# Kernel optimization log

Hardware: AMD Instinct MI355X
Metric: run time of the kernel (lower is better)

## Reference

```python
import jax, jax.numpy as jnp
from jax import lax
import numpy as np

# TopoLoss(dim=1, p=2, topo_lambda=1.0)
# p=2 -> Euclidean ground metric for the Vietoris-Rips filtration.
# This reference computes the dominant H0 persistence diagram of the VR complex:
# for a point cloud, H0 births are all 0 and deaths are exactly the MST edge
# weights (Kruskal/union-find == Prim, computed here with a fixed-length scan).
# Wasserstein distance between the two diagrams (equal cardinality N-1, births 0)
# reduces to optimal 1D matching of the sorted death values (q=1, the
# torch_topological WassersteinDistance default).
TOPO_LAMBDA = 1.0
EPS = 1e-12


def _pairwise_euclidean(x):
    # x: [B, N, D] -> [B, N, N] via the Gram trick (avoids [B,N,N,D] temp)
    sq = jnp.sum(x * x, axis=-1)                      # [B, N]
    g = jnp.einsum('bnd,bmd->bnm', x, x)              # [B, N, N]
    d2 = sq[:, :, None] + sq[:, None, :] - 2.0 * g
    return jnp.sqrt(jnp.maximum(d2, 0.0) + EPS)


def _mst_deaths(D):
    # Prim's algorithm on a dense distance matrix D: [N, N].
    # Returns the sorted MST edge weights = H0 death times ([N-1]).
    N = D.shape[0]
    inf = jnp.asarray(jnp.inf, D.dtype)
    in_tree0 = jnp.zeros((N,), bool).at[0].set(True)
    min_dist0 = D[0]

    def step(carry, _):
        in_tree, min_dist = carry
        masked = jnp.where(in_tree, inf, min_dist)
        j = jnp.argmin(masked)
        death = masked[j]
        in_tree = in_tree.at[j].set(True)
        min_dist = jnp.minimum(min_dist, D[j])
        return (in_tree, min_dist), death

    _, deaths = lax.scan(step, (in_tree0, min_dist0), None, length=N - 1)
    return jnp.sort(deaths)


def _h0_diagram_deaths(x):
    # x: [B, N, D] -> sorted death values [B, N-1]
    D = _pairwise_euclidean(x)
    return jax.vmap(_mst_deaths)(D)


def setup_inputs() -> dict:
    key = jax.random.key(0)
    k1, k2 = jax.random.split(key)
    B, N, D = 64, 1024, 3
    gts = jax.random.normal(k1, (B, N, D), dtype=jnp.float32)
    preds = jax.random.normal(k2, (B, N, D), dtype=jnp.float32)
    return {"gts": gts, "preds": preds}


def reference(gts, preds):
    # note: source names pers_info_pred = complex(gts) (vars swapped there);
    # Wasserstein is symmetric so ordering is irrelevant.
    deaths_a = _h0_diagram_deaths(gts)    # [B, N-1]
    deaths_b = _h0_diagram_deaths(preds)  # [B, N-1]
    # W1 between diagrams with equal cardinality and births==0:
    # optimal matching of sorted death coordinates.
    per_batch = jnp.sum(jnp.abs(deaths_a - deaths_b), axis=-1)  # [B]
    return per_batch.mean() * TOPO_LAMBDA
```

## Files before the change

### kernel.cpp

```cpp
#include <hip/hip_runtime.h>
#include <math.h>

#define N 1024
#define T 1024
#define HALF 512
#define PHASE_CAP 10
#define SWITCH 80

typedef float v2f __attribute__((ext_vector_type(2)));
typedef unsigned long long ull;

#define INF64 0xFFFFFFFFFFFFFFFFull
#define INF32 0xFFFFFFFFu

__device__ __forceinline__ unsigned umin32(unsigned a, unsigned b) { return a < b ? a : b; }
__device__ __forceinline__ unsigned umax32(unsigned a, unsigned b) { return a > b ? a : b; }
__device__ __forceinline__ int imin32(int a, int b) { return a < b ? a : b; }

__device__ __forceinline__ unsigned walk_root(const unsigned* parent, unsigned x) {
    unsigned prev = x, cur = parent[x];
    while (cur != prev) {
        unsigned nxt = parent[cur];
        if (nxt == prev) { cur = umin32(cur, prev); break; }
        prev = cur; cur = nxt;
    }
    return cur;
}

#define DPP_MIN_SHR(v, sh)                                                                   \
    do {                                                                                     \
        unsigned _t = (unsigned)__builtin_amdgcn_update_dpp(                                 \
            (int)0xFFFFFFFF, (int)(v), 0x110 | (sh), 0xF, 0xF, false);                       \
        (v) = umin32((v), _t);                                                               \
    } while (0)

__global__ __launch_bounds__(T) void scan1_kernel(const float* __restrict__ gts,
                                                  const float* __restrict__ preds,
                                                  unsigned* __restrict__ bests1) {
    __shared__ float4 p4[N];
    __shared__ unsigned pb8[8][HALF];
    const int t = threadIdx.x;
    const int cloud = blockIdx.x >> 1;
    const int nh = blockIdx.x & 1;
    const float* __restrict__ src = (cloud < 64 ? gts : preds) + (size_t)(cloud & 63) * N * 3;

    {
        float* stg = (float*)&pb8[0][0];
        if (t < 768) ((float4*)stg)[t] = ((const float4*)src)[t];
        __syncthreads();
        p4[t] = make_float4(stg[3 * t], stg[3 * t + 1], stg[3 * t + 2], 0.0f);
        __syncthreads();
    }

    const int q = t & 127;
    const int s = t >> 7;
    const int jbase = s << 7;
    const int n0 = nh * HALF + q;
    const int n1 = n0 + 128, n2 = n0 + 256, n3 = n0 + 384;
    const float4 a0 = p4[n0], a1 = p4[n1], a2 = p4[n2], a3 = p4[n3];
    const v2f axA = (v2f){a0.x, a1.x}, ayA = (v2f){a0.y, a1.y}, azA = (v2f){a0.z, a1.z};
    const v2f axB = (v2f){a2.x, a3.x}, ayB = (v2f){a2.y, a3.y}, azB = (v2f){a2.z, a3.z};
    unsigned b0 = INF32, b1 = INF32, b2 = INF32, b3 = INF32;
    #pragma unroll 4
    for (int jj = 0; jj < 128; jj += 2) {
        const int j = jbase + jj;
        const float4 qa = p4[j];
        const float4 qb = p4[j + 1];
        #define STEP1(QQ, JV)                                                           \
        {                                                                               \
            const v2f sxv = (v2f){QQ.x, QQ.x}, syv = (v2f){QQ.y, QQ.y},                 \
                      szv = (v2f){QQ.z, QQ.z};                                          \
            v2f dxA = axA - sxv, dyA = ayA - syv, dzA = azA - szv;                      \
            v2f eA = dxA * dxA;                                                         \
            eA = __builtin_elementwise_fma(dyA, dyA, eA);                               \
            eA = __builtin_elementwise_fma(dzA, dzA, eA);                               \
            v2f dxB = axB - sxv, dyB = ayB - syv, dzB = azB - szv;                      \
            v2f eB = dxB * dxB;                                                         \
            eB = __builtin_elementwise_fma(dyB, dyB, eB);                               \
            eB = __builtin_elementwise_fma(dzB, dzB, eB);                               \
            unsigned kk;                                                                \
            kk = (__float_as_uint(eA.x) & 0xFFFFF800u) | (unsigned)(JV);                \
            b0 = umin32(b0, ((JV) == n0) ? INF32 : kk);                                 \
            kk = (__float_as_uint(eA.y) & 0xFFFFF800u) | (unsigned)(JV);                \
            b1 = umin32(b1, ((JV) == n1) ? INF32 : kk);                                 \
            kk = (__float_as_uint(eB.x) & 0xFFFFF800u) | (unsigned)(JV);                \
            b2 = umin32(b2, ((JV) == n2) ? INF32 : kk);                                 \
            kk = (__float_as_uint(eB.y) & 0xFFFFF800u) | (unsigned)(JV);                \
            b3 = umin32(b3, ((JV) == n3) ? INF32 : kk);                                 \
        }
        STEP1(qa, j)
        STEP1(qb, j + 1)
        #undef STEP1
    }
    pb8[s][q] = b0; pb8[s][q + 128] = b1; pb8[s][q + 256] = b2; pb8[s][q + 384] = b3;
    __syncthreads();
    if (t < HALF) {
        unsigned best = umin32(umin32(pb8[0][t], pb8[1][t]), umin32(pb8[2][t], pb8[3][t]));
        best = umin32(best, umin32(umin32(pb8[4][t], pb8[5][t]), umin32(pb8[6][t], pb8[7][t])));
        bests1[(size_t)cloud * N + nh * HALF + t] = best;
    }
}

__global__ __launch_bounds__(T) void scan2_kernel(const float* __restrict__ gts,
                                                  const float* __restrict__ preds,
                                                  const unsigned* __restrict__ bests1,
                                                  unsigned* __restrict__ bests2) {
    __shared__ float4 p4[N];
    __shared__ unsigned cw[N];
    __shared__ unsigned parent[N];
    __shared__ unsigned pb8[8][HALF];
    const int t = threadIdx.x;
    const int cloud = blockIdx.x >> 1;
    const int nh = blockIdx.x & 1;
    const float* __restrict__ src = (cloud < 64 ? gts : preds) + (size_t)(cloud & 63) * N * 3;

    {
        float* stg = (float*)&pb8[0][0];
        if (t < 768) ((float4*)stg)[t] = ((const float4*)src)[t];
        __syncthreads();
        p4[t] = make_float4(stg[3 * t], stg[3 * t + 1], stg[3 * t + 2], 0.0f);
    }
    parent[t] = bests1[(size_t)cloud * N + t] & 0x3FFu;
    __syncthreads();
    {
        unsigned r = walk_root(parent, (unsigned)t);
        parent[t] = r;
        cw[t] = r;
    }
    __syncthreads();

    const int q = t & 127;
    const int s = t >> 7;
    const int jbase = s << 7;
    const int n0 = nh * HALF + q;
    const int n1 = n0 + 128, n2 = n0 + 256, n3 = n0 + 384;
    const unsigned c0 = cw[n0], c1 = cw[n1], c2 = cw[n2], c3 = cw[n3];
    const float4 a0 = p4[n0], a1 = p4[n1], a2 = p4[n2], a3 = p4[n3];
    const v2f axA = (v2f){a0.x, a1.x}, ayA = (v2f){a0.y, a1.y}, azA = (v2f){a0.z, a1.z};
    const v2f axB = (v2f){a2.x, a3.x}, ayB = (v2f){a2.y, a3.y}, azB = (v2f){a2.z, a3.z};
    unsigned b0 = INF32, b1 = INF32, b2 = INF32, b3 = INF32;
    #pragma unroll 4
    for (int jj = 0; jj < 128; jj += 2) {
        const int j = jbase + jj;
        const float4 qa = p4[j];
        const float4 qb = p4[j + 1];
        uint2 cj = *(const uint2*)&cw[j];
        #define STEP2(QQ, CJ, JV)                                                       \
        {                                                                               \
            const v2f sxv = (v2f){QQ.x, QQ.x}, syv = (v2f){QQ.y, QQ.y},                 \
                      szv = (v2f){QQ.z, QQ.z};                                          \
            v2f dxA = axA - sxv, dyA = ayA - syv, dzA = azA - szv;                      \
            v2f eA = dxA * dxA;                                                         \
            eA = __builtin_elementwise_fma(dyA, dyA, eA);                               \
            eA = __builtin_elementwise_fma(dzA, dzA, eA);                               \
            v2f dxB = axB - sxv, dyB = ayB - syv, dzB = azB - szv;                      \
            v2f eB = dxB * dxB;                                                         \
            eB = __builtin_elementwise_fma(dyB, dyB, eB);                               \
            eB = __builtin_elementwise_fma(dzB, dzB, eB);                               \
            unsigned kk;                                                                \
            kk = (__float_as_uint(eA.x) & 0xFFFFF800u) | (unsigned)(JV);                \
            b0 = umin32(b0, ((CJ) == c0) ? INF32 : kk);                                 \
            kk = (__float_as_uint(eA.y) & 0xFFFFF800u) | (unsigned)(JV);                \
            b1 = umin32(b1, ((CJ) == c1) ? INF32 : kk);                                 \
            kk = (__float_as_uint(eB.x) & 0xFFFFF800u) | (unsigned)(JV);                \
            b2 = umin32(b2, ((CJ) == c2) ? INF32 : kk);                                 \
            kk = (__float_as_uint(eB.y) & 0xFFFFF800u) | (unsigned)(JV);                \
            b3 = umin32(b3, ((CJ) == c3) ? INF32 : kk);                                 \
        }
        STEP2(qa, cj.x, j)
        STEP2(qb, cj.y, j + 1)
        #undef STEP2
    }
    pb8[s][q] = b0; pb8[s][q + 128] = b1; pb8[s][q + 256] = b2; pb8[s][q + 384] = b3;
    __syncthreads();
    if (t < HALF) {
        unsigned best = umin32(umin32(pb8[0][t], pb8[1][t]), umin32(pb8[2][t], pb8[3][t]));
        best = umin32(best, umin32(umin32(pb8[4][t], pb8[5][t]), umin32(pb8[6][t], pb8[7][t])));
        bests2[(size_t)cloud * N + nh * HALF + t] = best;
    }
}

__global__ __launch_bounds__(T) void final_kernel(const float* __restrict__ gts,
                                                  const float* __restrict__ preds,
                                                  float* __restrict__ ws,
                                                  const unsigned* __restrict__ bests1,
                                                  const unsigned* __restrict__ bests2,
                                                  int nPre) {
    __shared__ float4 pts[N];
    __shared__ float4 spts[N];
    __shared__ unsigned comp[N];
    __shared__ ull bestComp[N];
    __shared__ unsigned parent[N];
    __shared__ __align__(16) unsigned pb[2][N];
    __shared__ float deaths[N];
    __shared__ unsigned wsum[16];
    __shared__ int deathCount;

    const int t = threadIdx.x;
    const int blk = blockIdx.x;
    const float* __restrict__ src = (blk < 64 ? gts : preds) + (size_t)(blk & 63) * N * 3;

    {
        float* stg = (float*)&spts[0];
        if (t < 768) ((float4*)stg)[t] = ((const float4*)src)[t];
        __syncthreads();
        float x = stg[3 * t], y = stg[3 * t + 1], z = stg[3 * t + 2];
        pts[t] = make_float4(x, y, z, __uint_as_float((unsigned)t));
        comp[t] = (unsigned)t;
        parent[t] = (unsigned)t;
        deaths[t] = 0.0f;
        bestComp[t] = INF64;
    }
    if (t == 0) deathCount = 0;
    __syncthreads();

    const int n = t & (HALF - 1);
    const int h = t >> 9;
    const int n2 = n + HALF;
    const int jbase = h * HALF;
    float4 pA = pts[n], pB = pts[n2];
    const v2f pxv = (v2f){pA.x, pB.x};
    const v2f pyv = (v2f){pA.y, pB.y};
    const v2f pzv = (v2f){pA.z, pB.z};

    if (nPre >= 1) {
        unsigned b1 = bests1[(size_t)blk * N + t];
        unsigned j1 = b1 & 0x3FFu;
        unsigned e1 = b1 & 0xFFFFF800u;
        parent[t] = j1;
        __syncthreads();
        {
            unsigned p = j1;
            unsigned gp = parent[p];
            bool mutual = (gp == (unsigned)t);
            bool rec = !mutual || ((unsigned)t < p);
            float dval = rec ? sqrtf(__uint_as_float(e1) + 1e-12f) : 0.0f;
            ull m = __ballot(rec);
            int cnt = __popcll(m);
            int base = 0;
            if ((t & 63) == 0 && cnt) base = atomicAdd(&deathCount, cnt);
            base = __shfl(base, 0, 64);
            if (rec) {
                int idx = base + __popcll(m & ((1ull << (t & 63)) - 1ull));
                if (idx < N - 1) deaths[idx] = dval;
            }
        }
        __syncthreads();
        {
            unsigned r = walk_root(parent, (unsigned)t);
            parent[t] = r;
            comp[t] = r;
            pts[t].w = __uint_as_float(r);
        }
        __syncthreads();
    }

    if (nPre >= 2) {
        unsigned b2 = bests2[(size_t)blk * N + t];
        if (b2 != INF32) {
            unsigned j2 = b2 & 0x3FFu, e2 = b2 & 0xFFFFF800u;
            unsigned mn = umin32((unsigned)t, j2), mx = umax32((unsigned)t, j2);
            atomicMin(&bestComp[comp[t]], ((ull)e2 << 20) | (ull)((mn << 10) | mx));
        }
        __syncthreads();
        const unsigned c = (unsigned)t;
        const bool isRoot = (parent[c] == c);
        {
            ull bc = bestComp[c];
            if (isRoot && bc != INF64) {
                unsigned mn = (unsigned)((bc >> 10) & 0x3FFu);
                unsigned mx = (unsigned)(bc & 0x3FFu);
                unsigned cm = comp[mn];
                parent[c] = (cm == c) ? comp[mx] : cm;
            }
        }
        __syncthreads();
        {
            bool rec = false;
            float dval = 0.0f;
            unsigned p = parent[c];
            if (isRoot && p != c) {
                unsigned gp = parent[p];
                bool mutual = (gp == c);
                rec = !mutual || (c < p);
                if (rec) dval = sqrtf(__uint_as_float((unsigned)(bestComp[c] >> 20)) + 1e-12f);
            }
            ull m = __ballot(rec);
            int cnt = __popcll(m);
            int base = 0;
            if ((t & 63) == 0 && cnt) base = atomicAdd(&deathCount, cnt);
            base = __shfl(base, 0, 64);
            if (rec) {
                int idx = base + __popcll(m & ((1ull << (t & 63)) - 1ull));
                if (idx < N - 1) deaths[idx] = dval;
            }
        }
        __syncthreads();
        {
            unsigned r = walk_root(parent, c);
            parent[t] = r;
            unsigned nc = walk_root(parent, comp[t]);
            comp[t] = nc;
            pts[t].w = __uint_as_float(nc);
            bestComp[t] = INF64;
        }
        __syncthreads();
    }

    int phase = nPre;
    while (N - deathCount > (nPre ? SWITCH : 1) && phase < PHASE_CAP) {
        const unsigned c0 = comp[n], c1 = comp[n2];
        unsigned best0 = INF32, best1 = INF32;
        #pragma unroll 8
        for (int jj = 0; jj < HALF; ++jj) {
            int j = jbase + jj;
            float4 pj = pts[j];
            unsigned cj = __float_as_uint(pj.w);
            v2f dx = pxv - (v2f){pj.x, pj.x};
            v2f dy = pyv - (v2f){pj.y, pj.y};
            v2f dz = pzv - (v2f){pj.z, pj.z};
            v2f e = dx * dx;
            e = __builtin_elementwise_fma(dy, dy, e);
            e = __builtin_elementwise_fma(dz, dz, e);
            unsigned k0 = (__float_as_uint(e.x) & 0xFFFFF800u) | (unsigned)j;
            unsigned k1 = (__float_as_uint(e.y) & 0xFFFFF800u) | (unsigned)j;
            k0 = (cj == c0) ? INF32 : k0;
            k1 = (cj == c1) ? INF32 : k1;
            best0 = umin32(best0, k0);
            best1 = umin32(best1, k1);
        }
        pb[h][n] = best0;
        pb[h][n2] = best1;
        __syncthreads();
        if (h == 0) {
            #pragma unroll
            for (int s = 0; s < 2; ++s) {
                int m = s == 0 ? n : n2;
                unsigned fb = umin32(pb[0][m], pb[1][m]);
                if (fb != INF32) {
                    unsigned j = fb & 0x3FFu, e = fb & 0xFFFFF800u;
                    unsigned mn = umin32((unsigned)m, j), mx = umax32((unsigned)m, j);
                    ull key = ((ull)e << 20) | (ull)((mn << 10) | mx);
                    if (phase == 0) bestComp[m] = key;
                    else atomicMin(&bestComp[comp[m]], key);
                }
            }
        }
        __syncthreads();
        const unsigned c = (unsigned)t;
        const bool isRoot = (parent[c] == c);
        {
            ull bc = bestComp[c];
            if (isRoot && bc != INF64) {
                unsigned mn = (unsigned)((bc >> 10) & 0x3FFu);
                unsigned mx = (unsigned)(bc & 0x3FFu);
                unsigned cm = comp[mn];
                parent[c] = (cm == c) ? comp[mx] : cm;
            }
        }
        __syncthreads();
        {
            bool rec = false;
            float dval = 0.0f;
            unsigned p = parent[c];
            if (isRoot && p != c) {
                unsigned gp = parent[p];
                bool mutual = (gp == c);
                rec = !mutual || (c < p);
                if (rec) dval = sqrtf(__uint_as_float((unsigned)(bestComp[c] >> 20)) + 1e-12f);
            }
            ull m = __ballot(rec);
            int cnt = __popcll(m);
            int base = 0;
            if ((t & 63) == 0 && cnt) base = atomicAdd(&deathCount, cnt);
            base = __shfl(base, 0, 64);
            if (rec) {
                int idx = base + __popcll(m & ((1ull << (t & 63)) - 1ull));
                if (idx < N - 1) deaths[idx] = dval;
            }
        }
        __syncthreads();
        {
            unsigned r = walk_root(parent, c);
            parent[t] = r;
            unsigned nc = walk_root(parent, comp[t]);
            comp[t] = nc;
            pts[t].w = __uint_as_float(nc);
            bestComp[t] = INF64;
        }
        __syncthreads();
        ++phase;
    }

    const int dcbase = deathCount;
    const int comps = N - dcbase;
    if (comps > 1) {
        unsigned* scomp = &pb[0][0];
        unsigned* hist = &pb[1][0];
        unsigned* wavemin = &pb[1][0];
        uint2* segs = (uint2*)&bestComp[0];
        const int lane = t & 63;
        const int wid = t >> 6;

        hist[t] = 0;
        __syncthreads();
        atomicAdd(&hist[comp[t]], 1u);
        __syncthreads();
        unsigned cnt = hist[t];
        unsigned inc = cnt;
        #pragma unroll
        for (int d = 1; d < 64; d <<= 1) {
            unsigned u = __shfl_up(inc, d, 64);
            if (lane >= d) inc += u;
        }
        if (lane == 63) wsum[wid] = inc;
        __syncthreads();
        unsigned wof = 0;
        for (int i = 0; i < wid; ++i) wof += wsum[i];
        unsigned excl = wof + inc - cnt;
        if (cnt) { segs[t].x = excl; segs[t].y = excl + cnt; }
        __syncthreads();
        hist[t] = excl;
        __syncthreads();
        {
            unsigned pos = atomicAdd(&hist[comp[t]], 1u);
            spts[pos] = pts[t];
            scomp[pos] = comp[t];
        }
        __syncthreads();

        unsigned c_cur = comp[0];
        v2f pxv2 = (v2f){0.f, 0.f}, pyv2 = pxv2, pzv2 = pxv2;
        unsigned myc0 = 0, myc1 = 0, md0 = INF32, md1 = INF32;
        if (t < HALF) {
            float4 q0 = spts[t], q1 = spts[t + HALF];
            myc0 = scomp[t];
            myc1 = scomp[t + HALF];
            pxv2 = (v2f){q0.x, q1.x};
            pyv2 = (v2f){q0.y, q1.y};
            pzv2 = (v2f){q0.z, q1.z};
            if (myc0 == c_cur) pxv2.x = INFINITY;
            if (myc1 == c_cur) pxv2.y = INFINITY;
        }

        for (int step = 0; step < comps - 1; ++step) {
            if (t < HALF) {
                uint2 sg = segs[c_cur];
                const int jb = (int)sg.x, je = (int)sg.y, jl = je - 1;
                for (int base = jb; base < je; base += 4) {
                    float4 q0 = spts[base];
                    float4 q1 = spts[imin32(base + 1, jl)];
                    float4 q2 = spts[imin32(base + 2, jl)];
                    float4 q3 = spts[imin32(base + 3, jl)];
                    #define RELAX(qq)                                                        \
                        {                                                                    \
                            v2f dx = pxv2 - (v2f){qq.x, qq.x};                               \
                            v2f dy = pyv2 - (v2f){qq.y, qq.y};                               \
                            v2f dz = pzv2 - (v2f){qq.z, qq.z};                               \
                            v2f e = dx * dx;                                                 \
                            e = __builtin_elementwise_fma(dy, dy, e);                        \
                            e = __builtin_elementwise_fma(dz, dz, e);                        \
                            md0 = umin32(md0, (__float_as_uint(e.x) & 0xFFFFFC00u) | myc0);  \
                            md1 = umin32(md1, (__float_as_uint(e.y) & 0xFFFFFC00u) | myc1);  \
                        }
                    RELAX(q0) RELAX(q1) RELAX(q2) RELAX(q3)
                    #undef RELAX
                }
                unsigned v = umin32(md0, md1);
                DPP_MIN_SHR(v, 1);
                DPP_MIN_SHR(v, 2);
                DPP_MIN_SHR(v, 4);
                DPP_MIN_SHR(v, 8);
                unsigned r0 = (unsigned)__builtin_amdgcn_readlane((int)v, 15);
                unsigned r1 = (unsigned)__builtin_amdgcn_readlane((int)v, 31);
                unsigned r2 = (unsigned)__builtin_amdgcn_readlane((int)v, 47);
                unsigned r3 = (unsigned)__builtin_amdgcn_readlane((int)v, 63);
                if (lane == 0)
                    wavemin[(step & 1) * 8 + wid] = umin32(umin32(r0, r1), umin32(r2, r3));
            }
            __syncthreads();
            if (t < HALF) {
                const uint4* wmv = (const uint4*)(wavemin + (step & 1) * 8);
                uint4 u0 = wmv[0], u1 = wmv[1];
                unsigned m0 = umin32(umin32(u0.x, u0.y), umin32(u0.z, u0.w));
                unsigned m1 = umin32(umin32(u1.x, u1.y), umin32(u1.z, u1.w));
                unsigned G = umin32(m0, m1);
                c_cur = G & 0x3FFu;
                if (t == 0)
                    deaths[dcbase + step] = sqrtf(__uint_as_float(G & 0xFFFFFC00u) + 1e-12f);
                if (myc0 == c_cur) { pxv2.x = INFINITY; md0 = INF32; }
                if (myc1 == c_cur) { pxv2.y = INFINITY; md1 = INF32; }
            }
        }
    }

    if (t == 0) deaths[N - 1] = INFINITY;
    __syncthreads();
    {
        float v = deaths[t];
        #pragma unroll
        for (int k = 2; k <= N; k <<= 1) {
            const bool up = ((t & k) == 0);
            #pragma unroll
            for (int j = k >> 1; j > 0; j >>= 1) {
                float u;
                if (j >= 64) {
                    deaths[t] = v;
                    __syncthreads();
                    u = deaths[t ^ j];
                    __syncthreads();
                } else {
                    u = __shfl_xor(v, j, 64);
                }
                v = (((t & j) == 0) == up) ? fminf(v, u) : fmaxf(v, u);
            }
        }
        float* dst = ws + (size_t)blk * N;
        dst[t] = (t < N - 1) ? v : 0.0f;
    }
}

__global__ __launch_bounds__(256) void diff_kernel(const float* __restrict__ ws,
                                                   float* __restrict__ out) {
    __shared__ float red[4];
    const int t = threadIdx.x;
    const int b = blockIdx.x;
    const float* a = ws + (size_t)b * N;
    const float* c = ws + (size_t)(64 + b) * N;
    float sum = 0.0f;
    for (int i = t; i < N; i += 256)
        sum += fabsf(a[i] - c[i]);
    #pragma unroll
    for (int off = 32; off > 0; off >>= 1)
        sum += __shfl_down(sum, off, 64);
    if ((t & 63) == 0) red[t >> 6] = sum;
    __syncthreads();
    if (t == 0)
        atomicAdd(out, (red[0] + red[1] + red[2] + red[3]) * (1.0f / 64.0f));
}

extern "C" void kernel_launch(void* const* d_in, const int* in_sizes, int n_in,
                              void* d_out, int out_size, void* d_ws, size_t ws_size,
                              hipStream_t stream) {
    const float* gts = (const float*)d_in[0];
    const float* preds = (const float*)d_in[1];
    float* ws = (float*)d_ws;
    unsigned* bests1 = (unsigned*)d_ws;
    unsigned* bests2 = bests1 + 128 * N;
    const bool big = ws_size >= (size_t)(2u * 128u * N * 4u);

    if (big) {
        hipLaunchKernelGGL(scan1_kernel, dim3(256), dim3(T), 0, stream, gts, preds, bests1);
        hipLaunchKernelGGL(scan2_kernel, dim3(256), dim3(T), 0, stream, gts, preds, bests1, bests2);
        hipLaunchKernelGGL(final_kernel, dim3(128), dim3(T), 0, stream,
                           gts, preds, ws, bests1, bests2, 2);
    } else {
        hipLaunchKernelGGL(final_kernel, dim3(128), dim3(T), 0, stream,
                           gts, preds, ws, (const unsigned*)nullptr, (const unsigned*)nullptr, 0);
    }
    hipMemsetAsync(d_out, 0, sizeof(float), stream);
    hipLaunchKernelGGL(diff_kernel, dim3(64), dim3(256), 0, stream, ws, (float*)d_out);
}
```

Before: 218.2 us.

## Halve final kernel block to 512 threads, each handling two points

Shrinks final_kernel from 1024 to 512 threads per block, with each thread owning points t and t+512 across init, the Boruvka phases, the prefix scan and the bitonic sort. The sequential Prim tail previously left half the block idle. It now runs on all threads, and the j=512 sort stage becomes a register swap. The trade is fewer waves to hide latency in the O(N^2) Boruvka scans and longer per-thread loops, but block-wide barriers get cheaper.

```diff
diff --git a/kernel.cpp b/kernel.cpp
--- a/kernel.cpp
+++ b/kernel.cpp
@@ -3,6 +3,7 @@
 
 #define N 1024
 #define T 1024
+#define TF 512
 #define HALF 512
 #define PHASE_CAP 10
 #define SWITCH 80
@@ -180,12 +181,12 @@
     }
 }
 
-__global__ __launch_bounds__(T) void final_kernel(const float* __restrict__ gts,
-                                                  const float* __restrict__ preds,
-                                                  float* __restrict__ ws,
-                                                  const unsigned* __restrict__ bests1,
-                                                  const unsigned* __restrict__ bests2,
-                                                  int nPre) {
+__global__ __launch_bounds__(TF) void final_kernel(const float* __restrict__ gts,
+                                                   const float* __restrict__ preds,
+                                                   float* __restrict__ ws,
+                                                   const unsigned* __restrict__ bests1,
+                                                   const unsigned* __restrict__ bests2,
+                                                   int nPre) {
     __shared__ float4 pts[N];
     __shared__ float4 spts[N];
     __shared__ unsigned comp[N];
@@ -197,199 +198,231 @@
     __shared__ int deathCount;
 
     const int t = threadIdx.x;
+    const int tb = t + HALF;
     const int blk = blockIdx.x;
     const float* __restrict__ src = (blk < 64 ? gts : preds) + (size_t)(blk & 63) * N * 3;
 
     {
         float* stg = (float*)&spts[0];
-        if (t < 768) ((float4*)stg)[t] = ((const float4*)src)[t];
-        __syncthreads();
-        float x = stg[3 * t], y = stg[3 * t + 1], z = stg[3 * t + 2];
-        pts[t] = make_float4(x, y, z, __uint_as_float((unsigned)t));
-        comp[t] = (unsigned)t;
-        parent[t] = (unsigned)t;
-        deaths[t] = 0.0f;
-        bestComp[t] = INF64;
+        for (int i = t; i < 768; i += TF) ((float4*)stg)[i] = ((const float4*)src)[i];
+        __syncthreads();
+        #pragma unroll
+        for (int e = t; e < N; e += TF) {
+            float x = stg[3 * e], y = stg[3 * e + 1], z = stg[3 * e + 2];
+            pts[e] = make_float4(x, y, z, __uint_as_float((unsigned)e));
+            comp[e] = (unsigned)e;
+            parent[e] = (unsigned)e;
+            deaths[e] = 0.0f;
+            bestComp[e] = INF64;
+        }
     }
     if (t == 0) deathCount = 0;
     __syncthreads();
 
-    const int n = t & (HALF - 1);
-    const int h = t >> 9;
-    const int n2 = n + HALF;
-    const int jbase = h * HALF;
-    float4 pA = pts[n], pB = pts[n2];
-    const v2f pxv = (v2f){pA.x, pB.x};
-    const v2f pyv = (v2f){pA.y, pB.y};
-    const v2f pzv = (v2f){pA.z, pB.z};
-
     if (nPre >= 1) {
-        unsigned b1 = bests1[(size_t)blk * N + t];
-        unsigned j1 = b1 & 0x3FFu;
-        unsigned e1 = b1 & 0xFFFFF800u;
-        parent[t] = j1;
-        __syncthreads();
-        {
-            unsigned p = j1;
-            unsigned gp = parent[p];
-            bool mutual = (gp == (unsigned)t);
-            bool rec = !mutual || ((unsigned)t < p);
-            float dval = rec ? sqrtf(__uint_as_float(e1) + 1e-12f) : 0.0f;
-            ull m = __ballot(rec);
-            int cnt = __popcll(m);
+        unsigned bA = bests1[(size_t)blk * N + t];
+        unsigned bB = bests1[(size_t)blk * N + tb];
+        unsigned jA = bA & 0x3FFu, eAb = bA & 0xFFFFF800u;
+        unsigned jB = bB & 0x3FFu, eBb = bB & 0xFFFFF800u;
+        parent[t] = jA;
+        parent[tb] = jB;
+        __syncthreads();
+        {
+            unsigned gpA = parent[jA];
+            bool recA = !(gpA == (unsigned)t) || ((unsigned)t < jA);
+            float dvalA = recA ? sqrtf(__uint_as_float(eAb) + 1e-12f) : 0.0f;
+            unsigned gpB = parent[jB];
+            bool recB = !(gpB == (unsigned)tb) || ((unsigned)tb < jB);
+            float dvalB = recB ? sqrtf(__uint_as_float(eBb) + 1e-12f) : 0.0f;
+            ull mA = __ballot(recA), mB = __ballot(recB);
+            int cntA = __popcll(mA);
+            int cnt = cntA + __popcll(mB);
             int base = 0;
             if ((t & 63) == 0 && cnt) base = atomicAdd(&deathCount, cnt);
             base = __shfl(base, 0, 64);
-            if (rec) {
-                int idx = base + __popcll(m & ((1ull << (t & 63)) - 1ull));
-                if (idx < N - 1) deaths[idx] = dval;
-            }
+            ull below = (1ull << (t & 63)) - 1ull;
+            if (recA) { int idx = base + __popcll(mA & below); if (idx < N - 1) deaths[idx] = dvalA; }
+            if (recB) { int idx = base + cntA + __popcll(mB & below); if (idx < N - 1) deaths[idx] = dvalB; }
         }
         __syncthreads();
         {
             unsigned r = walk_root(parent, (unsigned)t);
-            parent[t] = r;
-            comp[t] = r;
-            pts[t].w = __uint_as_float(r);
+            parent[t] = r; comp[t] = r; pts[t].w = __uint_as_float(r);
+            unsigned r2 = walk_root(parent, (unsigned)tb);
+            parent[tb] = r2; comp[tb] = r2; pts[tb].w = __uint_as_float(r2);
         }
         __syncthreads();
     }
 
     if (nPre >= 2) {
-        unsigned b2 = bests2[(size_t)blk * N + t];
-        if (b2 != INF32) {
-            unsigned j2 = b2 & 0x3FFu, e2 = b2 & 0xFFFFF800u;
-            unsigned mn = umin32((unsigned)t, j2), mx = umax32((unsigned)t, j2);
-            atomicMin(&bestComp[comp[t]], ((ull)e2 << 20) | (ull)((mn << 10) | mx));
-        }
-        __syncthreads();
-        const unsigned c = (unsigned)t;
-        const bool isRoot = (parent[c] == c);
-        {
-            ull bc = bestComp[c];
-            if (isRoot && bc != INF64) {
-                unsigned mn = (unsigned)((bc >> 10) & 0x3FFu);
-                unsigned mx = (unsigned)(bc & 0x3FFu);
+        {
+            unsigned b2 = bests2[(size_t)blk * N + t];
+            if (b2 != INF32) {
+                unsigned j2 = b2 & 0x3FFu, e2 = b2 & 0xFFFFF800u;
+                unsigned mn = umin32((unsigned)t, j2), mx = umax32((unsigned)t, j2);
+                atomicMin(&bestComp[comp[t]], ((ull)e2 << 20) | (ull)((mn << 10) | mx));
+            }
+            b2 = bests2[(size_t)blk * N + tb];
+            if (b2 != INF32) {
+                unsigned j2 = b2 & 0x3FFu, e2 = b2 & 0xFFFFF800u;
+                unsigned mn = umin32((unsigned)tb, j2), mx = umax32((unsigned)tb, j2);
+                atomicMin(&bestComp[comp[tb]], ((ull)e2 << 20) | (ull)((mn << 10) | mx));
+            }
+        }
+        __syncthreads();
+        const bool isRootA = (parent[t] == (unsigned)t);
+        const bool isRootB = (parent[tb] == (unsigned)tb);
+        {
+            ull bc = bestComp[t];
+            if (isRootA && bc != INF64) {
+                unsigned mn = (unsigned)((bc >> 10) & 0x3FFu), mx = (unsigned)(bc & 0x3FFu);
                 unsigned cm = comp[mn];
-                parent[c] = (cm == c) ? comp[mx] : cm;
-            }
-        }
-        __syncthreads();
-        {
-            bool rec = false;
-            float dval = 0.0f;
-            unsigned p = parent[c];
-            if (isRoot && p != c) {
+                parent[t] = (cm == (unsigned)t) ? comp[mx] : cm;
+            }
+            bc = bestComp[tb];
+            if (isRootB && bc != INF64) {
+                unsigned mn = (unsigned)((bc >> 10) & 0x3FFu), mx = (unsigned)(bc & 0x3FFu);
+                unsigned cm = comp[mn];
+                parent[tb] = (cm == (unsigned)tb) ? comp[mx] : cm;
+            }
+        }
+        __syncthreads();
+        {
+            bool recA = false, recB = false;
+            float dvalA = 0.0f, dvalB = 0.0f;
+            unsigned p = parent[t];
+            if (isRootA && p != (unsigned)t) {
                 unsigned gp = parent[p];
-                bool mutual = (gp == c);
-                rec = !mutual || (c < p);
-                if (rec) dval = sqrtf(__uint_as_float((unsigned)(bestComp[c] >> 20)) + 1e-12f);
-            }
-            ull m = __ballot(rec);
-            int cnt = __popcll(m);
+                recA = !(gp == (unsigned)t) || ((unsigned)t < p);
+                if (recA) dvalA = sqrtf(__uint_as_float((unsigned)(bestComp[t] >> 20)) + 1e-12f);
+            }
+            p = parent[tb];
+            if (isRootB && p != (unsigned)tb) {
+                unsigned gp = parent[p];
+                recB = !(gp == (unsigned)tb) || ((unsigned)tb < p);
+                if (recB) dvalB = sqrtf(__uint_as_float((unsigned)(bestComp[tb] >> 20)) + 1e-12f);
+            }
+            ull mA = __ballot(recA), mB = __ballot(recB);
+            int cntA = __popcll(mA);
+            int cnt = cntA + __popcll(mB);
             int base = 0;
             if ((t & 63) == 0 && cnt) base = atomicAdd(&deathCount, cnt);
             base = __shfl(base, 0, 64);
-            if (rec) {
-                int idx = base + __popcll(m & ((1ull << (t & 63)) - 1ull));
-                if (idx < N - 1) deaths[idx] = dval;
-            }
-        }
-        __syncthreads();
-        {
-            unsigned r = walk_root(parent, c);
+            ull below = (1ull << (t & 63)) - 1ull;
+            if (recA) { int idx = base + __popcll(mA & below); if (idx < N - 1) deaths[idx] = dvalA; }
+            if (recB) { int idx = base + cntA + __popcll(mB & below); if (idx < N - 1) deaths[idx] = dvalB; }
+        }
+        __syncthreads();
+        {
+            unsigned r = walk_root(parent, (unsigned)t);
             parent[t] = r;
             unsigned nc = walk_root(parent, comp[t]);
-            comp[t] = nc;
-            pts[t].w = __uint_as_float(nc);
-            bestComp[t] = INF64;
-        }
-        __syncthreads();
-    }
-
-    int phase = nPre;
-    while (N - deathCount > (nPre ? SWITCH : 1) && phase < PHASE_CAP) {
-        const unsigned c0 = comp[n], c1 = comp[n2];
-        unsigned best0 = INF32, best1 = INF32;
-        #pragma unroll 8
-        for (int jj = 0; jj < HALF; ++jj) {
-            int j = jbase + jj;
-            float4 pj = pts[j];
-            unsigned cj = __float_as_uint(pj.w);
-            v2f dx = pxv - (v2f){pj.x, pj.x};
-            v2f dy = pyv - (v2f){pj.y, pj.y};
-            v2f dz = pzv - (v2f){pj.z, pj.z};
-            v2f e = dx * dx;
-            e = __builtin_elementwise_fma(dy, dy, e);
-            e = __builtin_elementwise_fma(dz, dz, e);
-            unsigned k0 = (__float_as_uint(e.x) & 0xFFFFF800u) | (unsigned)j;
-            unsigned k1 = (__float_as_uint(e.y) & 0xFFFFF800u) | (unsigned)j;
-            k0 = (cj == c0) ? INF32 : k0;
-            k1 = (cj == c1) ? INF32 : k1;
-            best0 = umin32(best0, k0);
-            best1 = umin32(best1, k1);
-        }
-        pb[h][n] = best0;
-        pb[h][n2] = best1;
-        __syncthreads();
-        if (h == 0) {
-            #pragma unroll
-            for (int s = 0; s < 2; ++s) {
-                int m = s == 0 ? n : n2;
-                unsigned fb = umin32(pb[0][m], pb[1][m]);
-                if (fb != INF32) {
-                    unsigned j = fb & 0x3FFu, e = fb & 0xFFFFF800u;
-                    unsigned mn = umin32((unsigned)m, j), mx = umax32((unsigned)m, j);
-                    ull key = ((ull)e << 20) | (ull)((mn << 10) | mx);
-                    if (phase == 0) bestComp[m] = key;
-                    else atomicMin(&bestComp[comp[m]], key);
+            comp[t] = nc; pts[t].w = __uint_as_float(nc); bestComp[t] = INF64;
+            r = walk_root(parent, (unsigned)tb);
+            parent[tb] = r;
+            nc = walk_root(parent, comp[tb]);
+            comp[tb] = nc; pts[tb].w = __uint_as_float(nc); bestComp[tb] = INF64;
+        }
+        __syncthreads();
+    }
+
+    {
+        float4 pA = pts[t], pB = pts[tb];
+        const v2f pxv = (v2f){pA.x, pB.x};
+        const v2f pyv = (v2f){pA.y, pB.y};
+        const v2f pzv = (v2f){pA.z, pB.z};
+        int phase = nPre;
+        while (N - deathCount > (nPre ? SWITCH : 1) && phase < PHASE_CAP) {
+            const unsigned c0 = comp[t], c1 = comp[tb];
+            unsigned best0 = INF32, best1 = INF32;
+            #pragma unroll 8
+            for (int j = 0; j < N; ++j) {
+                float4 pj = pts[j];
+                unsigned cj = __float_as_uint(pj.w);
+                v2f dx = pxv - (v2f){pj.x, pj.x};
+                v2f dy = pyv - (v2f){pj.y, pj.y};
+                v2f dz = pzv - (v2f){pj.z, pj.z};
+                v2f e = dx * dx;
+                e = __builtin_elementwise_fma(dy, dy, e);
+                e = __builtin_elementwise_fma(dz, dz, e);
+                unsigned k0 = (__float_as_uint(e.x) & 0xFFFFF800u) | (unsigned)j;
+                unsigned k1 = (__float_as_uint(e.y) & 0xFFFFF800u) | (unsigned)j;
+                k0 = (cj == c0) ? INF32 : k0;
+                k1 = (cj == c1) ? INF32 : k1;
+                best0 = umin32(best0, k0);
+                best1 = umin32(best1, k1);
+            }
+            if (best0 != INF32) {
+                unsigned j = best0 & 0x3FFu, e = best0 & 0xFFFFF800u;
+                unsigned mn = umin32((unsigned)t, j), mx = umax32((unsigned)t, j);
+                ull key = ((ull)e << 20) | (ull)((mn << 10) | mx);
+                if (phase == 0) bestComp[t] = key;
+                else atomicMin(&bestComp[comp[t]], key);
+            }
+            if (best1 != INF32) {
+                unsigned j = best1 & 0x3FFu, e = best1 & 0xFFFFF800u;
+                unsigned mn = umin32((unsigned)tb, j), mx = umax32((unsigned)tb, j);
+                ull key = ((ull)e << 20) | (ull)((mn << 10) | mx);
+                if (phase == 0) bestComp[tb] = key;
+                else atomicMin(&bestComp[comp[tb]], key);
+            }
+            __syncthreads();
+            const bool isRootA = (parent[t] == (unsigned)t);
+            const bool isRootB = (parent[tb] == (unsigned)tb);
+            {
+                ull bc = bestComp[t];
+                if (isRootA && bc != INF64) {
+                    unsigned mn = (unsigned)((bc >> 10) & 0x3FFu), mx = (unsigned)(bc & 0x3FFu);
+                    unsigned cm = comp[mn];
+                    parent[t] = (cm == (unsigned)t) ? comp[mx] : cm;
                 }
-            }
-        }
-        __syncthreads();
-        const unsigned c = (unsigned)t;
-        const bool isRoot = (parent[c] == c);
-        {
-            ull bc = bestComp[c];
-            if (isRoot && bc != INF64) {
-                unsigned mn = (unsigned)((bc >> 10) & 0x3FFu);
-                unsigned mx = (unsigned)(bc & 0x3FFu);
-                unsigned cm = comp[mn];
-                parent[c] = (cm == c) ? comp[mx] : cm;
-            }
-        }
-        __syncthreads();
-        {
-            bool rec = false;
-            float dval = 0.0f;
-            unsigned p = parent[c];
-            if (isRoot && p != c) {
-                unsigned gp = parent[p];
-                bool mutual = (gp == c);
-                rec = !mutual || (c < p);
-                if (rec) dval = sqrtf(__uint_as_float((unsigned)(bestComp[c] >> 20)) + 1e-12f);
-            }
-            ull m = __ballot(rec);
-            int cnt = __popcll(m);
-            int base = 0;
-            if ((t & 63) == 0 && cnt) base = atomicAdd(&deathCount, cnt);
-            base = __shfl(base, 0, 64);
-            if (rec) {
-                int idx = base + __popcll(m & ((1ull << (t & 63)) - 1ull));
-                if (idx < N - 1) deaths[idx] = dval;
-            }
-        }
-        __syncthreads();
-        {
-            unsigned r = walk_root(parent, c);
-            parent[t] = r;
-            unsigned nc = walk_root(parent, comp[t]);
-            comp[t] = nc;
-            pts[t].w = __uint_as_float(nc);
-            bestComp[t] = INF64;
-        }
-        __syncthreads();
-        ++phase;
+                bc = bestComp[tb];
+                if (isRootB && bc != INF64) {
+                    unsigned mn = (unsigned)((bc >> 10) & 0x3FFu), mx = (unsigned)(bc & 0x3FFu);
+                    unsigned cm = comp[mn];
+                    parent[tb] = (cm == (unsigned)tb) ? comp[mx] : cm;
+                }
+            }
+            __syncthreads();
+            {
+                bool recA = false, recB = false;
+                float dvalA = 0.0f, dvalB = 0.0f;
+                unsigned p = parent[t];
+                if (isRootA && p != (unsigned)t) {
+                    unsigned gp = parent[p];
+                    recA = !(gp == (unsigned)t) || ((unsigned)t < p);
+                    if (recA) dvalA = sqrtf(__uint_as_float((unsigned)(bestComp[t] >> 20)) + 1e-12f);
+                }
+                p = parent[tb];
+                if (isRootB && p != (unsigned)tb) {
+                    unsigned gp = parent[p];
+                    recB = !(gp == (unsigned)tb) || ((unsigned)tb < p);
+                    if (recB) dvalB = sqrtf(__uint_as_float((unsigned)(bestComp[tb] >> 20)) + 1e-12f);
+                }
+                ull mA = __ballot(recA), mB = __ballot(recB);
+                int cntA = __popcll(mA);
+                int cnt = cntA + __popcll(mB);
+                int base = 0;
+                if ((t & 63) == 0 && cnt) base = atomicAdd(&deathCount, cnt);
+                base = __shfl(base, 0, 64);
+                ull below = (1ull << (t & 63)) - 1ull;
+                if (recA) { int idx = base + __popcll(mA & below); if (idx < N - 1) deaths[idx] = dvalA; }
+                if (recB) { int idx = base + cntA + __popcll(mB & below); if (idx < N - 1) deaths[idx] = dvalB; }
+            }
+            __syncthreads();
+            {
+                unsigned r = walk_root(parent, (unsigned)t);
+                parent[t] = r;
+                unsigned nc = walk_root(parent, comp[t]);
+                comp[t] = nc; pts[t].w = __uint_as_float(nc); bestComp[t] = INF64;
+                r = walk_root(parent, (unsigned)tb);
+                parent[tb] = r;
+                nc = walk_root(parent, comp[tb]);
+                comp[tb] = nc; pts[tb].w = __uint_as_float(nc); bestComp[tb] = INF64;
+            }
+            __syncthreads();
+            ++phase;
+        }
     }
 
     const int dcbase = deathCount;
@@ -402,40 +435,50 @@
         const int lane = t & 63;
         const int wid = t >> 6;
 
-        hist[t] = 0;
+        hist[t] = 0; hist[tb] = 0;
         __syncthreads();
         atomicAdd(&hist[comp[t]], 1u);
-        __syncthreads();
-        unsigned cnt = hist[t];
-        unsigned inc = cnt;
+        atomicAdd(&hist[comp[tb]], 1u);
+        __syncthreads();
+        unsigned cA = hist[t], cB = hist[tb];
+        unsigned incA = cA, incB = cB;
         #pragma unroll
         for (int d = 1; d < 64; d <<= 1) {
-            unsigned u = __shfl_up(inc, d, 64);
-            if (lane >= d) inc += u;
-        }
-        if (lane == 63) wsum[wid] = inc;
-        __syncthreads();
-        unsigned wof = 0;
-        for (int i = 0; i < wid; ++i) wof += wsum[i];
-        unsigned excl = wof + inc - cnt;
-        if (cnt) { segs[t].x = excl; segs[t].y = excl + cnt; }
-        __syncthreads();
-        hist[t] = excl;
+            unsigned uA = __shfl_up(incA, d, 64);
+            unsigned uB = __shfl_up(incB, d, 64);
+            if (lane >= d) { incA += uA; incB += uB; }
+        }
+        if (lane == 63) { wsum[wid] = incA; wsum[8 + wid] = incB; }
+        __syncthreads();
+        unsigned wofA = 0, totA = 0, wofB = 0;
+        for (int i = 0; i < 8; ++i) {
+            unsigned w = wsum[i];
+            if (i < wid) wofA += w;
+            totA += w;
+        }
+        for (int i = 0; i < wid; ++i) wofB += wsum[8 + i];
+        unsigned exclA = wofA + incA - cA;
+        unsigned exclB = totA + wofB + incB - cB;
+        if (cA) { segs[t].x = exclA; segs[t].y = exclA + cA; }
+        if (cB) { segs[tb].x = exclB; segs[tb].y = exclB + cB; }
+        __syncthreads();
+        hist[t] = exclA; hist[tb] = exclB;
         __syncthreads();
         {
             unsigned pos = atomicAdd(&hist[comp[t]], 1u);
-            spts[pos] = pts[t];
-            scomp[pos] = comp[t];
+            spts[pos] = pts[t]; scomp[pos] = comp[t];
+            pos = atomicAdd(&hist[comp[tb]], 1u);
+            spts[pos] = pts[tb]; scomp[pos] = comp[tb];
         }
         __syncthreads();
 
         unsigned c_cur = comp[0];
         v2f pxv2 = (v2f){0.f, 0.f}, pyv2 = pxv2, pzv2 = pxv2;
         unsigned myc0 = 0, myc1 = 0, md0 = INF32, md1 = INF32;
-        if (t < HALF) {
-            float4 q0 = spts[t], q1 = spts[t + HALF];
+        {
+            float4 q0 = spts[t], q1 = spts[tb];
             myc0 = scomp[t];
-            myc1 = scomp[t + HALF];
+            myc1 = scomp[tb];
             pxv2 = (v2f){q0.x, q1.x};
             pyv2 = (v2f){q0.y, q1.y};
             pzv2 = (v2f){q0.z, q1.z};
@@ -444,7 +487,7 @@
         }
 
         for (int step = 0; step < comps - 1; ++step) {
-            if (t < HALF) {
+            {
                 uint2 sg = segs[c_cur];
                 const int jb = (int)sg.x, je = (int)sg.y, jl = je - 1;
                 for (int base = jb; base < je; base += 4) {
@@ -479,7 +522,7 @@
                     wavemin[(step & 1) * 8 + wid] = umin32(umin32(r0, r1), umin32(r2, r3));
             }
             __syncthreads();
-            if (t < HALF) {
+            {
                 const uint4* wmv = (const uint4*)(wavemin + (step & 1) * 8);
                 uint4 u0 = wmv[0], u1 = wmv[1];
                 unsigned m0 = umin32(umin32(u0.x, u0.y), umin32(u0.z, u0.w));
@@ -494,29 +537,35 @@
         }
     }
 
-    if (t == 0) deaths[N - 1] = INFINITY;
-    __syncthreads();
     {
-        float v = deaths[t];
+        float v0 = deaths[t], v1 = deaths[tb];
+        if (t == TF - 1) v1 = INFINITY;
         #pragma unroll
         for (int k = 2; k <= N; k <<= 1) {
-            const bool up = ((t & k) == 0);
             #pragma unroll
             for (int j = k >> 1; j > 0; j >>= 1) {
-                float u;
-                if (j >= 64) {
-                    deaths[t] = v;
+                const bool up0 = ((t & k) == 0);
+                const bool up1 = ((tb & k) == 0);
+                float u0, u1;
+                if (j == 512) {
+                    u0 = v1; u1 = v0;
+                } else if (j >= 64) {
+                    deaths[t] = v0; deaths[tb] = v1;
                     __syncthreads();
-                    u = deaths[t ^ j];
+                    u0 = deaths[t ^ j];
+                    u1 = deaths[tb ^ j];
                     __syncthreads();
                 } else {
-                    u = __shfl_xor(v, j, 64);
+                    u0 = __shfl_xor(v0, j, 64);
+                    u1 = __shfl_xor(v1, j, 64);
                 }
-                v = (((t & j) == 0) == up) ? fminf(v, u) : fmaxf(v, u);
+                v0 = (((t & j) == 0) == up0) ? fminf(v0, u0) : fmaxf(v0, u0);
+                v1 = (((tb & j) == 0) == up1) ? fminf(v1, u1) : fmaxf(v1, u1);
             }
         }
         float* dst = ws + (size_t)blk * N;
-        dst[t] = (t < N - 1) ? v : 0.0f;
+        dst[t] = v0;
+        dst[tb] = (tb < N - 1) ? v1 : 0.0f;
     }
 }
 
@@ -552,10 +601,10 @@
     if (big) {
         hipLaunchKernelGGL(scan1_kernel, dim3(256), dim3(T), 0, stream, gts, preds, bests1);
         hipLaunchKernelGGL(scan2_kernel, dim3(256), dim3(T), 0, stream, gts, preds, bests1, bests2);
-        hipLaunchKernelGGL(final_kernel, dim3(128), dim3(T), 0, stream,
+        hipLaunchKernelGGL(final_kernel, dim3(128), dim3(TF), 0, stream,
                            gts, preds, ws, bests1, bests2, 2);
     } else {
-        hipLaunchKernelGGL(final_kernel, dim3(128), dim3(T), 0, stream,
+        hipLaunchKernelGGL(final_kernel, dim3(128), dim3(TF), 0, stream,
                            gts, preds, ws, (const unsigned*)nullptr, (const unsigned*)nullptr, 0);
     }
     hipMemsetAsync(d_out, 0, sizeof(float), stream);
```

Measured after the change: 213.5 us. -2.2%, faster.
